# Performance work log

Hardware: AMD Instinct MI355X
Metric: run time of the kernel (lower is better)

## Reference

```python
import jax, jax.numpy as jnp
import numpy as np

N, D, H = 8192, 1024, 256

def setup_inputs() -> dict:
    key = jax.random.key(0)
    ks = jax.random.split(key, 11)
    s = lambda fan_in: 1.0 / np.sqrt(fan_in)
    return {
        "x": jax.random.normal(ks[0], (N, D), dtype=jnp.float32),
        "lin1_w": jax.random.uniform(ks[1], (H, D), jnp.float32, -s(D), s(D)),
        "lin1_b": jax.random.uniform(ks[2], (H,), jnp.float32, -s(D), s(D)),
        "q_w": jax.random.uniform(ks[3], (H, H), jnp.float32, -s(H), s(H)),
        "q_b": jax.random.uniform(ks[4], (H,), jnp.float32, -s(H), s(H)),
        "k_w": jax.random.uniform(ks[5], (H, H), jnp.float32, -s(H), s(H)),
        "k_b": jax.random.uniform(ks[6], (H,), jnp.float32, -s(H), s(H)),
        "v_w": jax.random.uniform(ks[7], (H, H), jnp.float32, -s(H), s(H)),
        "v_b": jax.random.uniform(ks[8], (H,), jnp.float32, -s(H), s(H)),
        "lin2_w": jax.random.uniform(ks[9], (1, H), jnp.float32, -s(H), s(H)),
        "lin2_b": jax.random.uniform(ks[10], (1,), jnp.float32, -s(H), s(H)),
    }

def reference(x, lin1_w, lin1_b, q_w, q_b, k_w, k_b, v_w, v_b, lin2_w, lin2_b):
    h = x @ lin1_w.T + lin1_b                      # [N, H]
    q = h @ q_w.T + q_b                            # [N, H]
    k = h @ k_w.T + k_b                            # [N, H]
    v = h @ v_w.T + v_b                            # [N, H]
    scale = 1.0 / np.sqrt(H).astype(np.float32)
    w = (q @ k.T) * scale                          # [N, N] dense scores
    a = jax.nn.softmax(w, axis=-1)                 # row softmax
    h = h + a @ v                                  # residual
    out = h @ lin2_w.T + lin2_b                    # [N, 1]
    return out.squeeze(-1)                         # [N]
```

## Files before the change

### kernel.cpp

```cpp
#include <hip/hip_runtime.h>
#include <hip/hip_bf16.h>
#include <math.h>

typedef __attribute__((ext_vector_type(4))) float f32x4;
typedef __attribute__((ext_vector_type(8))) short bf16x8;

#define N_TOK 8192
#define D_IN  1024
#define H_DIM 256
#define S_SPLIT 16
#define QSCALE 0.09016844f

static __device__ __forceinline__ float bf2f(unsigned short u) {
  return __uint_as_float(((unsigned)u) << 16);
}
static __device__ __forceinline__ float fast_exp2(float x) {
  float e;
  asm("v_exp_f32 %0, %1" : "=v"(e) : "v"(x));
  return e;
}
static __device__ __forceinline__ void gload_lds16(const void* g, void* l) {
  __builtin_amdgcn_global_load_lds(
      (const __attribute__((address_space(1))) void*)g,
      (__attribute__((address_space(3))) void*)l, 16, 0, 0);
}
#define QLOAD(dst, base, off) \
  asm volatile("global_load_dwordx4 %0, %1, off offset:" #off \
               : "=v"(dst) : "v"(base))

__global__ __launch_bounds__(256) void prep_kernel(
    const float* __restrict__ w1, const float* __restrict__ qw,
    const float* __restrict__ kw, const float* __restrict__ vw,
    const float* __restrict__ vb, const float* __restrict__ w2,
    __hip_bfloat16* __restrict__ w1b, __hip_bfloat16* __restrict__ qwb,
    __hip_bfloat16* __restrict__ kwb, float* __restrict__ wv2, float* __restrict__ bv2)
{
  int b = blockIdx.x, tid = threadIdx.x;
  if (b < 384) {
    const float* in; __hip_bfloat16* out; int base;
    if (b < 256)      { in = w1; out = w1b; base = b; }
    else if (b < 320) { in = qw; out = qwb; base = b - 256; }
    else              { in = kw; out = kwb; base = b - 320; }
    int i = base * 1024 + tid * 4;
    float4 v = *reinterpret_cast<const float4*>(in + i);
    union { __hip_bfloat16 h[4]; ushort4 u; } cv;
    cv.h[0] = __float2bfloat16(v.x);
    cv.h[1] = __float2bfloat16(v.y);
    cv.h[2] = __float2bfloat16(v.z);
    cv.h[3] = __float2bfloat16(v.w);
    *reinterpret_cast<ushort4*>(out + i) = cv.u;
    return;
  }
  if (b < 392) {
    __shared__ float sw2b[256];
    __shared__ float red2[8][32];
    sw2b[tid] = w2[tid];
    __syncthreads();
    const int jb = (b - 384) * 32;
    const int jj = tid & 31, cg = tid >> 5;
    float a = 0.f;
    #pragma unroll 8
    for (int c = cg * 32; c < cg * 32 + 32; ++c)
      a = fmaf(vw[c * 256 + jb + jj], sw2b[c], a);
    red2[cg][jj] = a;
    __syncthreads();
    if (tid < 32) {
      float s = 0.f;
      #pragma unroll
      for (int g = 0; g < 8; ++g) s += red2[g][tid];
      wv2[jb + tid] = s;
    }
    return;
  }
  __shared__ float red[256];
  red[tid] = vb[tid] * w2[tid];
  __syncthreads();
  for (int s = 128; s > 0; s >>= 1) {
    if (tid < s) red[tid] += red[tid + s];
    __syncthreads();
  }
  if (tid == 0) bv2[0] = red[0];
}

__global__ __launch_bounds__(512) void front_kernel(
    const float* __restrict__ x, const __hip_bfloat16* __restrict__ W1,
    const __hip_bfloat16* __restrict__ Wq, const __hip_bfloat16* __restrict__ Wk,
    const float* __restrict__ b1, const float* __restrict__ bq, const float* __restrict__ bk,
    const float* __restrict__ w2, const float* __restrict__ wv2, const float* __restrict__ b2,
    __hip_bfloat16* __restrict__ Qo, __hip_bfloat16* __restrict__ Ko,
    float* __restrict__ hw2, float* __restrict__ vs)
{
  __shared__ __attribute__((aligned(16))) unsigned char lds[73728];
  const int tid = threadIdx.x;
  const int w = tid >> 6, l = tid & 63, r16 = l & 15, kg = l >> 4;
  const int rowbase = blockIdx.x * 16;
  const int rsw8 = (r16 & 7) << 4;
  const char* W1b = (const char*)W1;

  {
    const int xrow = tid >> 5;
    const int xcb  = (tid & 31) * 64;
    const float* xp = x + (size_t)(rowbase + xrow) * D_IN + (tid & 31) * 32;
    f32x4 xr[8];
    #pragma unroll
    for (int i = 0; i < 8; ++i) xr[i] = *reinterpret_cast<const f32x4*>(xp + i * 4);
    #pragma unroll
    for (int i = 0; i < 4; ++i) {
      union { __hip_bfloat16 h[8]; uint4 u; } cv;
      #pragma unroll
      for (int e = 0; e < 4; ++e) {
        cv.h[e]     = __float2bfloat16(xr[2 * i][e]);
        cv.h[4 + e] = __float2bfloat16(xr[2 * i + 1][e]);
      }
      *reinterpret_cast<uint4*>(&lds[xrow * 2048 + ((xcb + i * 16) ^ ((xrow & 7) << 4))]) = cv.u;
    }
  }

  f32x4 acc[2];
  acc[0] = (f32x4){0.f, 0.f, 0.f, 0.f};
  acc[1] = (f32x4){0.f, 0.f, 0.f, 0.f};

  #pragma unroll
  for (int i = 0; i < 2; ++i) {
    int p = i * 8192 + tid * 16;
    int col = p >> 6, bb = p & 63;
    gload_lds16(W1b + (size_t)col * 2048 + (bb ^ ((col & 3) << 4)), &lds[32768 + p]);
  }
  __syncthreads();

  for (int t = 0; t < 32; ++t) {
    const int cur = t & 1;
    if (t + 1 < 32) {
      #pragma unroll
      for (int i = 0; i < 2; ++i) {
        int p = i * 8192 + tid * 16;
        int col = p >> 6, bb = p & 63;
        gload_lds16(W1b + (size_t)col * 2048 + (t + 1) * 64 + (bb ^ ((col & 3) << 4)),
                    &lds[32768 + (cur ^ 1) * 16384 + p]);
      }
    }
    const unsigned char* Wc = &lds[32768 + cur * 16384];
    bf16x8 a = *reinterpret_cast<const bf16x8*>(
        &lds[r16 * 2048 + ((t * 64 + kg * 16) ^ rsw8)]);
    #pragma unroll
    for (int c = 0; c < 2; ++c) {
      const int colloc = w * 32 + c * 16 + r16;
      bf16x8 b = *reinterpret_cast<const bf16x8*>(
          Wc + colloc * 64 + ((kg * 16) ^ ((colloc & 3) << 4)));
      acc[c] = __builtin_amdgcn_mfma_f32_16x16x32_bf16(a, b, acc[c], 0, 0, 0);
    }
    __syncthreads();
  }

  #pragma unroll
  for (int c = 0; c < 2; ++c) {
    int col = w * 32 + c * 16 + r16;
    float bs = b1[col];
    #pragma unroll
    for (int j = 0; j < 4; ++j) {
      int row = kg * 4 + j;
      *reinterpret_cast<__hip_bfloat16*>(
          &lds[65536 + row * 512 + ((col * 2) ^ ((row & 7) << 4))]) =
          __float2bfloat16(acc[c][j] + bs);
    }
  }

  const char* wqB = (const char*)Wq;
  const char* wkB = (const char*)Wk;
  #pragma unroll
  for (int i = 0; i < 4; ++i) {
    int p = i * 8192 + tid * 16;
    int col = p >> 7, bb = p & 127;
    gload_lds16(wqB + (size_t)col * 512 + (bb ^ ((col & 7) << 4)), &lds[p]);
  }
  __syncthreads();

  f32x4 qacc[2];
  qacc[0] = (f32x4){0.f, 0.f, 0.f, 0.f};
  qacc[1] = (f32x4){0.f, 0.f, 0.f, 0.f};

  for (int r = 0; r < 8; ++r) {
    const int bufoff = (r & 1) ? 32768 : 0;
    if (r + 1 < 8) {
      const char* Wsel = (r + 1 < 4) ? wqB : wkB;
      const int kq1 = (r + 1) & 3;
      #pragma unroll
      for (int i = 0; i < 4; ++i) {
        int p = i * 8192 + tid * 16;
        int col = p >> 7, bb = p & 127;
        gload_lds16(Wsel + (size_t)col * 512 + kq1 * 128 + (bb ^ ((col & 7) << 4)),
                    &lds[(bufoff ^ 32768) + p]);
      }
    }
    const int kq = r & 3;
    const unsigned char* WT = &lds[bufoff];
    #pragma unroll
    for (int ks = 0; ks < 2; ++ks) {
      bf16x8 a = *reinterpret_cast<const bf16x8*>(
          &lds[65536 + r16 * 512 + ((kq * 128 + ks * 64 + kg * 16) ^ rsw8)]);
      #pragma unroll
      for (int c = 0; c < 2; ++c) {
        const int colloc = w * 32 + c * 16 + r16;
        bf16x8 b = *reinterpret_cast<const bf16x8*>(
            WT + colloc * 128 + ((ks * 64 + kg * 16) ^ ((colloc & 7) << 4)));
        qacc[c] = __builtin_amdgcn_mfma_f32_16x16x32_bf16(a, b, qacc[c], 0, 0, 0);
      }
    }
    if (r == 3) {
      #pragma unroll
      for (int c = 0; c < 2; ++c) {
        int col = w * 32 + c * 16 + r16;
        float bb = bq[col];
        #pragma unroll
        for (int j = 0; j < 4; ++j) {
          int row = rowbase + kg * 4 + j;
          Qo[(size_t)row * H_DIM + col] = __float2bfloat16((qacc[c][j] + bb) * QSCALE);
        }
        qacc[c] = (f32x4){0.f, 0.f, 0.f, 0.f};
      }
    }
    __syncthreads();
  }
  #pragma unroll
  for (int c = 0; c < 2; ++c) {
    int col = w * 32 + c * 16 + r16;
    float bb = bk[col];
    #pragma unroll
    for (int j = 0; j < 4; ++j) {
      int row = rowbase + kg * 4 + j;
      Ko[(size_t)row * H_DIM + col] = __float2bfloat16(qacc[c][j] + bb);
    }
  }

  {
    const bool isw2 = (w < 4);
    const float* wsel = isw2 ? w2 : wv2;
    const int c16 = l & 15;
    const int row = (w & 3) * 4 + (l >> 4);
    const int rs2 = (row & 7) << 4;
    bf16x8 h0 = *reinterpret_cast<const bf16x8*>(&lds[65536 + row * 512 + ((c16 * 32) ^ rs2)]);
    bf16x8 h1 = *reinterpret_cast<const bf16x8*>(&lds[65536 + row * 512 + ((c16 * 32 + 16) ^ rs2)]);
    float s = 0.f;
    #pragma unroll
    for (int i = 0; i < 8; ++i) s += bf2f((unsigned short)h0[i]) * wsel[c16 * 16 + i];
    #pragma unroll
    for (int i = 0; i < 8; ++i) s += bf2f((unsigned short)h1[i]) * wsel[c16 * 16 + 8 + i];
    #pragma unroll
    for (int off = 1; off < 16; off <<= 1) s += __shfl_xor(s, off);
    if (c16 == 0) {
      if (isw2) hw2[rowbase + row] = s + b2[0];
      else      vs[rowbase + row]  = s;
    }
  }
}

#define KVBLK 64
#define KRANGE (N_TOK / S_SPLIT)
__global__ __launch_bounds__(256, 2) void attn_partial_kernel(
    const __hip_bfloat16* __restrict__ Q, const __hip_bfloat16* __restrict__ K,
    const float* __restrict__ vsg, float* __restrict__ pden, float* __restrict__ pacc)
{
  __shared__ __attribute__((aligned(16))) unsigned char ktile[2][KVBLK * 512];
  __shared__ float vs_lds[KRANGE];

  const int tid = threadIdx.x;
  const int w   = tid >> 6;
  const int l   = tid & 63;
  const int r16 = l & 15;
  const int kg  = l >> 4;
  const int split   = blockIdx.y;
  const int mstart  = split * KRANGE;
  const int rowbase = blockIdx.x * 256 + w * 64;

  if (tid < KRANGE / 4)
    *reinterpret_cast<float4*>(vs_lds + tid * 4) =
        *reinterpret_cast<const float4*>(vsg + mstart + tid * 4);

  bf16x8 qf[4][8];
  #pragma unroll
  for (int sub = 0; sub < 4; ++sub) {
    const char* qp = (const char*)(Q + (size_t)(rowbase + sub * 16 + r16) * H_DIM + kg * 8);
    QLOAD(qf[sub][0], qp, 0);
    QLOAD(qf[sub][1], qp, 64);
    QLOAD(qf[sub][2], qp, 128);
    QLOAD(qf[sub][3], qp, 192);
    QLOAD(qf[sub][4], qp, 256);
    QLOAD(qf[sub][5], qp, 320);
    QLOAD(qf[sub][6], qp, 384);
    QLOAD(qf[sub][7], qp, 448);
  }
  asm volatile("s_waitcnt vmcnt(0)" ::: "memory");

  const int trow = tid >> 5;
  const int tbsw = ((tid & 31) * 16) ^ ((trow & 7) << 4);
  const char* kbase = (const char*)K + (size_t)(mstart + trow) * 512 + tbsw;
  const int ldst = trow * 512 + (tid & 31) * 16;

  const int rsw = (r16 & 7) << 4;
  const int cb  = kg * 16;

  float den[4][4], acc[4][4];
  #pragma unroll
  for (int sub = 0; sub < 4; ++sub)
    #pragma unroll
    for (int j = 0; j < 4; ++j) { den[sub][j] = 0.f; acc[sub][j] = 0.f; }

  #pragma unroll
  for (int i = 0; i < 8; ++i)
    gload_lds16(kbase + (size_t)(i * 8) * 512, &ktile[0][i * 4096 + ldst]);
  __syncthreads();

  const int NT = KRANGE / KVBLK;
  for (int t = 0; t < NT; ++t) {
    const int cur = t & 1;
    if (t + 1 < NT) {
      #pragma unroll
      for (int i = 0; i < 8; ++i)
        gload_lds16(kbase + (size_t)((t + 1) * KVBLK + i * 8) * 512,
                    &ktile[cur ^ 1][i * 4096 + ldst]);
    }

    const unsigned char* kt = &ktile[cur][0];
    #pragma unroll
    for (int h = 0; h < 2; ++h) {
      f32x4 d[4][2];
      #pragma unroll
      for (int sub = 0; sub < 4; ++sub)
        #pragma unroll
        for (int n = 0; n < 2; ++n) d[sub][n] = (f32x4){0.f, 0.f, 0.f, 0.f};

      __builtin_amdgcn_s_setprio(1);
      #pragma unroll
      for (int n = 0; n < 2; ++n) {
        const int row = h * 32 + n * 16 + r16;
        #pragma unroll
        for (int kk = 0; kk < 8; ++kk) {
          bf16x8 b = *reinterpret_cast<const bf16x8*>(
              kt + row * 512 + ((kk * 64 + cb) ^ rsw));
          d[0][n] = __builtin_amdgcn_mfma_f32_16x16x32_bf16(qf[0][kk], b, d[0][n], 0, 0, 0);
          d[1][n] = __builtin_amdgcn_mfma_f32_16x16x32_bf16(qf[1][kk], b, d[1][n], 0, 0, 0);
          d[2][n] = __builtin_amdgcn_mfma_f32_16x16x32_bf16(qf[2][kk], b, d[2][n], 0, 0, 0);
          d[3][n] = __builtin_amdgcn_mfma_f32_16x16x32_bf16(qf[3][kk], b, d[3][n], 0, 0, 0);
        }
      }
      __builtin_amdgcn_s_setprio(0);

      const float vsm0 = vs_lds[t * KVBLK + h * 32 + r16];
      const float vsm1 = vs_lds[t * KVBLK + h * 32 + 16 + r16];
      #pragma unroll
      for (int sub = 0; sub < 4; ++sub)
        #pragma unroll
        for (int j = 0; j < 4; ++j) {
          float e0 = fast_exp2(d[sub][0][j]);
          float e1 = fast_exp2(d[sub][1][j]);
          den[sub][j] += e0 + e1;
          acc[sub][j] = fmaf(e0, vsm0, fmaf(e1, vsm1, acc[sub][j]));
        }
    }
    __syncthreads();
  }

  #pragma unroll
  for (int sub = 0; sub < 4; ++sub)
    #pragma unroll
    for (int j = 0; j < 4; ++j) {
      #pragma unroll
      for (int off = 1; off < 16; off <<= 1) {
        den[sub][j] += __shfl_xor(den[sub][j], off);
        acc[sub][j] += __shfl_xor(acc[sub][j], off);
      }
    }
  if (r16 == 0) {
    #pragma unroll
    for (int sub = 0; sub < 4; ++sub)
      #pragma unroll
      for (int j = 0; j < 4; ++j) {
        int row = rowbase + sub * 16 + kg * 4 + j;
        pden[split * N_TOK + row] = den[sub][j];
        pacc[split * N_TOK + row] = acc[sub][j];
      }
  }
}

__global__ __launch_bounds__(256) void combine_kernel(
    const float* __restrict__ pden, const float* __restrict__ pacc,
    const float* __restrict__ hw2, const float* __restrict__ bv2, float* __restrict__ out)
{
  int r = blockIdx.x * 256 + threadIdx.x;
  float den = 0.f, acc = 0.f;
  #pragma unroll
  for (int s = 0; s < S_SPLIT; ++s) {
    den += pden[s * N_TOK + r];
    acc += pacc[s * N_TOK + r];
  }
  out[r] = hw2[r] + acc / den + bv2[0];
}

extern "C" void kernel_launch(void* const* d_in, const int* in_sizes, int n_in,
                              void* d_out, int out_size, void* d_ws, size_t ws_size,
                              hipStream_t stream) {
  const float* x      = (const float*)d_in[0];
  const float* lin1_w = (const float*)d_in[1];
  const float* lin1_b = (const float*)d_in[2];
  const float* q_w    = (const float*)d_in[3];
  const float* q_b    = (const float*)d_in[4];
  const float* k_w    = (const float*)d_in[5];
  const float* k_b    = (const float*)d_in[6];
  const float* v_w    = (const float*)d_in[7];
  const float* v_b    = (const float*)d_in[8];
  const float* lin2_w = (const float*)d_in[9];
  const float* lin2_b = (const float*)d_in[10];
  float* out = (float*)d_out;

  char* ws = (char*)d_ws;
  size_t off = 0;
  auto alloc = [&](size_t bytes) {
    char* p = ws + off;
    off += (bytes + 255) & ~(size_t)255;
    return p;
  };
  __hip_bfloat16* w1b = (__hip_bfloat16*)alloc((size_t)H_DIM * D_IN * 2);
  __hip_bfloat16* qwb = (__hip_bfloat16*)alloc((size_t)H_DIM * H_DIM * 2);
  __hip_bfloat16* kwb = (__hip_bfloat16*)alloc((size_t)H_DIM * H_DIM * 2);
  __hip_bfloat16* qb  = (__hip_bfloat16*)alloc((size_t)N_TOK * H_DIM * 2);
  __hip_bfloat16* kb  = (__hip_bfloat16*)alloc((size_t)N_TOK * H_DIM * 2);
  float* hw2  = (float*)alloc((size_t)N_TOK * 4);
  float* vsv  = (float*)alloc((size_t)N_TOK * 4);
  float* wv2  = (float*)alloc((size_t)H_DIM * 4);
  float* bv2  = (float*)alloc(256);
  float* pden = (float*)alloc((size_t)S_SPLIT * N_TOK * 4);
  float* pacc = (float*)alloc((size_t)S_SPLIT * N_TOK * 4);
  (void)ws_size; (void)in_sizes; (void)n_in; (void)out_size;

  prep_kernel<<<393, 256, 0, stream>>>(lin1_w, q_w, k_w, v_w, v_b, lin2_w,
                                       w1b, qwb, kwb, wv2, bv2);

  front_kernel<<<N_TOK / 16, 512, 0, stream>>>(x, w1b, qwb, kwb, lin1_b, q_b, k_b,
                                               lin2_w, wv2, lin2_b, qb, kb, hw2, vsv);

  attn_partial_kernel<<<dim3(32, S_SPLIT), 256, 0, stream>>>(qb, kb, vsv, pden, pacc);

  combine_kernel<<<N_TOK / 256, 256, 0, stream>>>(pden, pacc, hw2, bv2, out);
}
```

Baseline: 82.07 us.

## Restructure front kernel to 32-row tiles with direct register loads of weights

The front kernel now processes 32 rows per block instead of 16. The LDS staging of x and W1 is replaced by direct global loads into registers, with conversion to bf16 just before the MFMAs. The Q and K projections now run concurrently on separate wave groups, each wave covering 64 output columns across two row tiles, so the double-buffered LDS loop and most block barriers go away. LDS use drops to the h tile only, which should allow more blocks per CU. In exchange, weight reads go straight from global memory through cache without coalesced LDS staging, and register pressure per wave rises.

```diff
diff --git a/kernel.cpp b/kernel.cpp
--- a/kernel.cpp
+++ b/kernel.cpp
@@ -90,166 +90,144 @@
     __hip_bfloat16* __restrict__ Qo, __hip_bfloat16* __restrict__ Ko,
     float* __restrict__ hw2, float* __restrict__ vs)
 {
-  __shared__ __attribute__((aligned(16))) unsigned char lds[73728];
+  __shared__ __attribute__((aligned(16))) unsigned char h_lds[32 * 512];
   const int tid = threadIdx.x;
   const int w = tid >> 6, l = tid & 63, r16 = l & 15, kg = l >> 4;
-  const int rowbase = blockIdx.x * 16;
+  const int wr = w >> 2, wc = w & 3;
+  const int rowbase = blockIdx.x * 32;
   const int rsw8 = (r16 & 7) << 4;
-  const char* W1b = (const char*)W1;
 
   {
-    const int xrow = tid >> 5;
-    const int xcb  = (tid & 31) * 64;
-    const float* xp = x + (size_t)(rowbase + xrow) * D_IN + (tid & 31) * 32;
-    f32x4 xr[8];
-    #pragma unroll
-    for (int i = 0; i < 8; ++i) xr[i] = *reinterpret_cast<const f32x4*>(xp + i * 4);
-    #pragma unroll
-    for (int i = 0; i < 4; ++i) {
-      union { __hip_bfloat16 h[8]; uint4 u; } cv;
-      #pragma unroll
-      for (int e = 0; e < 4; ++e) {
-        cv.h[e]     = __float2bfloat16(xr[2 * i][e]);
-        cv.h[4 + e] = __float2bfloat16(xr[2 * i + 1][e]);
-      }
-      *reinterpret_cast<uint4*>(&lds[xrow * 2048 + ((xcb + i * 16) ^ ((xrow & 7) << 4))]) = cv.u;
-    }
-  }
-
-  f32x4 acc[2];
-  acc[0] = (f32x4){0.f, 0.f, 0.f, 0.f};
-  acc[1] = (f32x4){0.f, 0.f, 0.f, 0.f};
-
-  #pragma unroll
-  for (int i = 0; i < 2; ++i) {
-    int p = i * 8192 + tid * 16;
-    int col = p >> 6, bb = p & 63;
-    gload_lds16(W1b + (size_t)col * 2048 + (bb ^ ((col & 3) << 4)), &lds[32768 + p]);
+    const char* xb  = (const char*)(x + (size_t)(rowbase + wr * 16 + r16) * D_IN);
+    const char* w1r = (const char*)W1;
+
+    f32x4 acc[4];
+    #pragma unroll
+    for (int c = 0; c < 4; ++c) acc[c] = (f32x4){0.f, 0.f, 0.f, 0.f};
+
+    for (int chunk = 0; chunk < 8; ++chunk) {
+      f32x4 xa[8];
+      #pragma unroll
+      for (int ks = 0; ks < 4; ++ks) {
+        xa[2 * ks]     = *reinterpret_cast<const f32x4*>(xb + chunk * 512 + ks * 128 + kg * 32);
+        xa[2 * ks + 1] = *reinterpret_cast<const f32x4*>(xb + chunk * 512 + ks * 128 + kg * 32 + 16);
+      }
+      bf16x8 bw[4][4];
+      #pragma unroll
+      for (int ks = 0; ks < 4; ++ks)
+        #pragma unroll
+        for (int c = 0; c < 4; ++c)
+          bw[ks][c] = *reinterpret_cast<const bf16x8*>(
+              w1r + (size_t)(wc * 64 + c * 16 + r16) * 2048 + chunk * 256 + ks * 64 + kg * 16);
+      #pragma unroll
+      for (int ks = 0; ks < 4; ++ks) {
+        union { __hip_bfloat16 h[8]; bf16x8 v; } af;
+        #pragma unroll
+        for (int e = 0; e < 4; ++e) {
+          af.h[e]     = __float2bfloat16(xa[2 * ks][e]);
+          af.h[4 + e] = __float2bfloat16(xa[2 * ks + 1][e]);
+        }
+        #pragma unroll
+        for (int c = 0; c < 4; ++c)
+          acc[c] = __builtin_amdgcn_mfma_f32_16x16x32_bf16(af.v, bw[ks][c], acc[c], 0, 0, 0);
+      }
+    }
+
+    #pragma unroll
+    for (int c = 0; c < 4; ++c) {
+      int col = wc * 64 + c * 16 + r16;
+      float bs = b1[col];
+      #pragma unroll
+      for (int j = 0; j < 4; ++j) {
+        int row = wr * 16 + kg * 4 + j;
+        *reinterpret_cast<__hip_bfloat16*>(
+            &h_lds[row * 512 + ((col * 2) ^ ((row & 7) << 4))]) =
+            __float2bfloat16(acc[c][j] + bs);
+      }
+    }
   }
   __syncthreads();
 
-  for (int t = 0; t < 32; ++t) {
-    const int cur = t & 1;
-    if (t + 1 < 32) {
-      #pragma unroll
-      for (int i = 0; i < 2; ++i) {
-        int p = i * 8192 + tid * 16;
-        int col = p >> 6, bb = p & 63;
-        gload_lds16(W1b + (size_t)col * 2048 + (t + 1) * 64 + (bb ^ ((col & 3) << 4)),
-                    &lds[32768 + (cur ^ 1) * 16384 + p]);
-      }
-    }
-    const unsigned char* Wc = &lds[32768 + cur * 16384];
-    bf16x8 a = *reinterpret_cast<const bf16x8*>(
-        &lds[r16 * 2048 + ((t * 64 + kg * 16) ^ rsw8)]);
-    #pragma unroll
-    for (int c = 0; c < 2; ++c) {
-      const int colloc = w * 32 + c * 16 + r16;
-      bf16x8 b = *reinterpret_cast<const bf16x8*>(
-          Wc + colloc * 64 + ((kg * 16) ^ ((colloc & 3) << 4)));
-      acc[c] = __builtin_amdgcn_mfma_f32_16x16x32_bf16(a, b, acc[c], 0, 0, 0);
-    }
-    __syncthreads();
-  }
-
-  #pragma unroll
-  for (int c = 0; c < 2; ++c) {
-    int col = w * 32 + c * 16 + r16;
-    float bs = b1[col];
-    #pragma unroll
-    for (int j = 0; j < 4; ++j) {
-      int row = kg * 4 + j;
-      *reinterpret_cast<__hip_bfloat16*>(
-          &lds[65536 + row * 512 + ((col * 2) ^ ((row & 7) << 4))]) =
-          __float2bfloat16(acc[c][j] + bs);
-    }
-  }
-
-  const char* wqB = (const char*)Wq;
-  const char* wkB = (const char*)Wk;
-  #pragma unroll
-  for (int i = 0; i < 4; ++i) {
-    int p = i * 8192 + tid * 16;
-    int col = p >> 7, bb = p & 127;
-    gload_lds16(wqB + (size_t)col * 512 + (bb ^ ((col & 7) << 4)), &lds[p]);
-  }
-  __syncthreads();
-
-  f32x4 qacc[2];
-  qacc[0] = (f32x4){0.f, 0.f, 0.f, 0.f};
-  qacc[1] = (f32x4){0.f, 0.f, 0.f, 0.f};
-
-  for (int r = 0; r < 8; ++r) {
-    const int bufoff = (r & 1) ? 32768 : 0;
-    if (r + 1 < 8) {
-      const char* Wsel = (r + 1 < 4) ? wqB : wkB;
-      const int kq1 = (r + 1) & 3;
-      #pragma unroll
-      for (int i = 0; i < 4; ++i) {
-        int p = i * 8192 + tid * 16;
-        int col = p >> 7, bb = p & 127;
-        gload_lds16(Wsel + (size_t)col * 512 + kq1 * 128 + (bb ^ ((col & 7) << 4)),
-                    &lds[(bufoff ^ 32768) + p]);
-      }
-    }
-    const int kq = r & 3;
-    const unsigned char* WT = &lds[bufoff];
-    #pragma unroll
-    for (int ks = 0; ks < 2; ++ks) {
-      bf16x8 a = *reinterpret_cast<const bf16x8*>(
-          &lds[65536 + r16 * 512 + ((kq * 128 + ks * 64 + kg * 16) ^ rsw8)]);
-      #pragma unroll
-      for (int c = 0; c < 2; ++c) {
-        const int colloc = w * 32 + c * 16 + r16;
-        bf16x8 b = *reinterpret_cast<const bf16x8*>(
-            WT + colloc * 128 + ((ks * 64 + kg * 16) ^ ((colloc & 7) << 4)));
-        qacc[c] = __builtin_amdgcn_mfma_f32_16x16x32_bf16(a, b, qacc[c], 0, 0, 0);
-      }
-    }
-    if (r == 3) {
-      #pragma unroll
-      for (int c = 0; c < 2; ++c) {
-        int col = w * 32 + c * 16 + r16;
-        float bb = bq[col];
+  {
+    const bool isq = (w < 4);
+    const char* Wp = (const char*)(isq ? Wq : Wk);
+    const int cb = (w & 3) * 64;
+
+    f32x4 qacc[2][4];
+    #pragma unroll
+    for (int rt = 0; rt < 2; ++rt)
+      #pragma unroll
+      for (int c = 0; c < 4; ++c) qacc[rt][c] = (f32x4){0.f, 0.f, 0.f, 0.f};
+
+    #pragma unroll
+    for (int half = 0; half < 2; ++half) {
+      bf16x8 bw2[4][4];
+      #pragma unroll
+      for (int ks = 0; ks < 4; ++ks)
+        #pragma unroll
+        for (int c = 0; c < 4; ++c)
+          bw2[ks][c] = *reinterpret_cast<const bf16x8*>(
+              Wp + (size_t)(cb + c * 16 + r16) * 512 + half * 256 + ks * 64 + kg * 16);
+      bf16x8 af2[2][4];
+      #pragma unroll
+      for (int rt = 0; rt < 2; ++rt)
+        #pragma unroll
+        for (int ks = 0; ks < 4; ++ks)
+          af2[rt][ks] = *reinterpret_cast<const bf16x8*>(
+              &h_lds[(rt * 16 + r16) * 512 + ((half * 256 + ks * 64 + kg * 16) ^ rsw8)]);
+      #pragma unroll
+      for (int ks = 0; ks < 4; ++ks)
+        #pragma unroll
+        for (int c = 0; c < 4; ++c) {
+          qacc[0][c] = __builtin_amdgcn_mfma_f32_16x16x32_bf16(af2[0][ks], bw2[ks][c], qacc[0][c], 0, 0, 0);
+          qacc[1][c] = __builtin_amdgcn_mfma_f32_16x16x32_bf16(af2[1][ks], bw2[ks][c], qacc[1][c], 0, 0, 0);
+        }
+    }
+
+    const float* bp = isq ? bq : bk;
+    const float scl = isq ? QSCALE : 1.f;
+    __hip_bfloat16* Op = isq ? Qo : Ko;
+    #pragma unroll
+    for (int rt = 0; rt < 2; ++rt)
+      #pragma unroll
+      for (int c = 0; c < 4; ++c) {
+        int col = cb + c * 16 + r16;
+        float bb = bp[col];
         #pragma unroll
         for (int j = 0; j < 4; ++j) {
-          int row = rowbase + kg * 4 + j;
-          Qo[(size_t)row * H_DIM + col] = __float2bfloat16((qacc[c][j] + bb) * QSCALE);
+          int row = rowbase + rt * 16 + kg * 4 + j;
+          Op[(size_t)row * H_DIM + col] = __float2bfloat16((qacc[rt][c][j] + bb) * scl);
         }
-        qacc[c] = (f32x4){0.f, 0.f, 0.f, 0.f};
-      }
-    }
-    __syncthreads();
-  }
-  #pragma unroll
-  for (int c = 0; c < 2; ++c) {
-    int col = w * 32 + c * 16 + r16;
-    float bb = bk[col];
-    #pragma unroll
-    for (int j = 0; j < 4; ++j) {
-      int row = rowbase + kg * 4 + j;
-      Ko[(size_t)row * H_DIM + col] = __float2bfloat16(qacc[c][j] + bb);
-    }
+      }
   }
 
   {
-    const bool isw2 = (w < 4);
-    const float* wsel = isw2 ? w2 : wv2;
     const int c16 = l & 15;
-    const int row = (w & 3) * 4 + (l >> 4);
+    const int row = w * 4 + (l >> 4);
     const int rs2 = (row & 7) << 4;
-    bf16x8 h0 = *reinterpret_cast<const bf16x8*>(&lds[65536 + row * 512 + ((c16 * 32) ^ rs2)]);
-    bf16x8 h1 = *reinterpret_cast<const bf16x8*>(&lds[65536 + row * 512 + ((c16 * 32 + 16) ^ rs2)]);
-    float s = 0.f;
-    #pragma unroll
-    for (int i = 0; i < 8; ++i) s += bf2f((unsigned short)h0[i]) * wsel[c16 * 16 + i];
-    #pragma unroll
-    for (int i = 0; i < 8; ++i) s += bf2f((unsigned short)h1[i]) * wsel[c16 * 16 + 8 + i];
-    #pragma unroll
-    for (int off = 1; off < 16; off <<= 1) s += __shfl_xor(s, off);
+    bf16x8 h0 = *reinterpret_cast<const bf16x8*>(&h_lds[row * 512 + ((c16 * 32) ^ rs2)]);
+    bf16x8 h1 = *reinterpret_cast<const bf16x8*>(&h_lds[row * 512 + ((c16 * 32 + 16) ^ rs2)]);
+    float s2 = 0.f, sv = 0.f;
+    #pragma unroll
+    for (int i = 0; i < 8; ++i) {
+      float hv = bf2f((unsigned short)h0[i]);
+      s2 += hv * w2[c16 * 16 + i];
+      sv += hv * wv2[c16 * 16 + i];
+    }
+    #pragma unroll
+    for (int i = 0; i < 8; ++i) {
+      float hv = bf2f((unsigned short)h1[i]);
+      s2 += hv * w2[c16 * 16 + 8 + i];
+      sv += hv * wv2[c16 * 16 + 8 + i];
+    }
+    #pragma unroll
+    for (int off = 1; off < 16; off <<= 1) {
+      s2 += __shfl_xor(s2, off);
+      sv += __shfl_xor(sv, off);
+    }
     if (c16 == 0) {
-      if (isw2) hw2[rowbase + row] = s + b2[0];
-      else      vs[rowbase + row]  = s;
+      hw2[rowbase + row] = s2 + b2[0];
+      vs[rowbase + row]  = sv;
     }
   }
 }
@@ -435,7 +413,7 @@
   prep_kernel<<<393, 256, 0, stream>>>(lin1_w, q_w, k_w, v_w, v_b, lin2_w,
                                        w1b, qwb, kwb, wv2, bv2);
 
-  front_kernel<<<N_TOK / 16, 512, 0, stream>>>(x, w1b, qwb, kwb, lin1_b, q_b, k_b,
+  front_kernel<<<N_TOK / 32, 512, 0, stream>>>(x, w1b, qwb, kwb, lin1_b, q_b, k_b,
                                                lin2_w, wv2, lin2_b, qb, kb, hw2, vsv);
 
   attn_partial_kernel<<<dim3(32, S_SPLIT), 256, 0, stream>>>(qb, kb, vsv, pden, pacc);
```

New measurement: 104.9 us. 1.28x slower.
